# Optimization experiments

Measured on AMD Instinct MI355X. Metric: run time of the kernel, lower is better.

Reference implementation:

```python
import jax, jax.numpy as jnp
import numpy as np

SHRINKAGE = 0.1  # matches init_kwargs shrinkage_rate


def setup_inputs() -> dict:
    key = jax.random.key(0)
    k0, k1, k2, k3 = jax.random.split(key, 4)
    B, F, T, D, P = 8192, 256, 32, 6, 8
    N = 2 ** D - 1  # internal nodes per tree
    L = 2 ** D      # leaves per tree
    return {
        "x": jax.random.normal(k0, (B, F), dtype=jnp.float32),
        "W": jax.random.normal(k1, (T, N, F), dtype=jnp.float32) / np.float32(np.sqrt(F)),
        "b": jax.random.normal(k2, (T, N), dtype=jnp.float32) * 0.01,
        "phi": jax.random.normal(k3, (T, L, P), dtype=jnp.float32),
    }


def reference(x, W, b, phi):
    # x: [B,F]; W: [T,N,F]; b: [T,N]; phi: [T,L,P]
    T, N, F = W.shape
    L = N + 1
    D = int(round(np.log2(L)))
    # all node gating probabilities in one batched GEMM: p(right) per internal node
    s = jax.nn.sigmoid(jnp.einsum('bf,tnf->btn', x, W) + b)  # [B,T,N]
    # heap (level-order) node indexing: node at level d with prefix q has index 2^d-1+q;
    # leaf l's bit at level d is (l >> (D-1-d)) & 1 (1 -> right child -> prob s, 0 -> 1-s)
    leaves = np.arange(L)
    leaf_prob = jnp.ones(s.shape[:2] + (L,), dtype=s.dtype)  # [B,T,L]
    for d in range(D):  # static small loop over tree depth
        bits = jnp.asarray((leaves >> (D - 1 - d)) & 1, dtype=bool)
        idx = (2 ** d - 1) + (leaves >> (D - d))
        sd = s[:, :, idx]  # [B,T,L]
        leaf_prob = leaf_prob * jnp.where(bits, sd, 1.0 - sd)
    # per-tree prediction = sum_l path_prob_l * phi_l; GBM output = shrinkage * sum_t
    tree_pred = jnp.einsum('btl,tlp->btp', leaf_prob, phi)  # [B,T,P]
    return SHRINKAGE * tree_pred.sum(axis=1)  # [B,P]
```

## Files before the change

kernel.cpp:

```cpp
#include <hip/hip_runtime.h>

#define B_TOT   8192
#define F_DIM   256
#define T_TREES 32
#define N_NODES 63
#define P_DIM   8
#define BM      128
#define SHRINK  0.1f

typedef __bf16 bf16_t;
typedef bf16_t bf16x8 __attribute__((ext_vector_type(8)));
typedef float  f32x4  __attribute__((ext_vector_type(4)));
typedef unsigned short ushort8_t __attribute__((ext_vector_type(8)));
typedef unsigned short ushort4_t __attribute__((ext_vector_type(4)));

__device__ __forceinline__ unsigned short f2bf(float f) {
    unsigned int u = __float_as_uint(f);
    u += 0x7fffu + ((u >> 16) & 1u);
    return (unsigned short)(u >> 16);
}
__device__ __forceinline__ unsigned int pk2bf(float a, float b) {
    unsigned int ua = __float_as_uint(a); ua += 0x7fffu + ((ua >> 16) & 1u);
    unsigned int ub = __float_as_uint(b); ub += 0x7fffu + ((ub >> 16) & 1u);
    return (ua >> 16) | (ub & 0xffff0000u);
}
__device__ __forceinline__ void gl_lds16(const void* g, void* l) {
    __builtin_amdgcn_global_load_lds(
        (const __attribute__((address_space(1))) unsigned int*)g,
        (__attribute__((address_space(3))) unsigned int*)l, 16, 0, 0);
}

__global__ __launch_bounds__(256) void cvt_all(
    const float* __restrict__ x, const float* __restrict__ W,
    const float* __restrict__ phi,
    unsigned short* __restrict__ xb, unsigned short* __restrict__ Wb,
    unsigned short* __restrict__ phiB, float* __restrict__ out)
{
    const int bx  = blockIdx.x;
    const int tid = threadIdx.x;
    if (bx < 2048) {
        const int i = bx * 256 + tid;
        const float4 v = *(const float4*)&x[(size_t)i * 4];
        ushort4_t h;
        h.x = f2bf(v.x); h.y = f2bf(v.y); h.z = f2bf(v.z); h.w = f2bf(v.w);
        *(ushort4_t*)&xb[(size_t)i * 4] = h;
    } else if (bx < 2560) {
        const int i = (bx - 2048) * 256 + tid;
        const int tree = i >> 12;
        const int rem  = i & 4095;
        const int row  = rem >> 6;
        const int c4   = rem & 63;
        float4 v = make_float4(0.f, 0.f, 0.f, 0.f);
        if (row < N_NODES)
            v = *(const float4*)&W[((size_t)(tree * N_NODES + row)) * F_DIM + c4 * 4];
        ushort4_t h;
        h.x = f2bf(v.x); h.y = f2bf(v.y); h.z = f2bf(v.z); h.w = f2bf(v.w);
        *(ushort4_t*)&Wb[(size_t)i * 4] = h;
    } else if (bx < 2576) {
        const int i = (bx - 2560) * 256 + tid;
        const int tree = i >> 7;
        const int rem  = i & 127;
        const int k2   = rem >> 6;
        const int lane = rem & 63;
        const int lm   = lane & 15;
        const int quad = lane >> 4;
        ushort8_t h;
#pragma unroll
        for (int j = 0; j < 8; ++j) {
            float v = 0.f;
            if (lm < 8) v = phi[(size_t)tree * 512 + (k2 * 32 + quad * 8 + j) * 8 + lm];
            h[j] = f2bf(v);
        }
        *(ushort8_t*)&phiB[(size_t)i * 8] = h;
    } else {
        const int i = (bx - 2576) * 256 + tid;
        *(float4*)&out[(size_t)i * 4] = make_float4(0.f, 0.f, 0.f, 0.f);
    }
}

__global__ __launch_bounds__(256, 4) void softgbm_main(
    const unsigned short* __restrict__ xb, const unsigned short* __restrict__ Wb,
    const unsigned short* __restrict__ phiB, const float* __restrict__ bias,
    float* __restrict__ out)
{
    __shared__ union Smem {
        struct { unsigned short A[BM * 64]; unsigned short B[BM * 64]; } g;
        unsigned short ss[2 * BM * 64];
    } sm;
    __shared__ float bs2[2][64];

    const int tid  = threadIdx.x;
    const int tp   = blockIdx.x;
    const int b0   = blockIdx.y * BM;
    const int wave = tid >> 6;
    const int lane = tid & 63;
    const int quad = lane >> 4;
    const int lm   = lane & 15;
    const int wr   = wave >> 1;
    const int wc   = wave & 1;

    if (tid < 128) {
        const int p = tid >> 6, node = tid & 63;
        bs2[p][node] = (node < N_NODES) ? bias[(tp * 2 + p) * N_NODES + node] : 0.f;
    }

    f32x4 acc[4][4];
#pragma unroll
    for (int m = 0; m < 4; ++m)
#pragma unroll
        for (int n = 0; n < 4; ++n)
            acc[m][n] = f32x4{0.f, 0.f, 0.f, 0.f};

    for (int ko = 0; ko < F_DIM; ko += 64) {
        __syncthreads();
#pragma unroll
        for (int i = 0; i < 4; ++i) {
            const int r = wave * 32 + i * 8 + (lane >> 3);
            const int c = (lane & 7) ^ (r & 7);
            gl_lds16(&xb[(size_t)(b0 + r) * F_DIM + ko + c * 8],
                     &sm.g.A[(wave * 32 + i * 8) * 64]);
        }
#pragma unroll
        for (int i = 0; i < 4; ++i) {
            const int r = wave * 32 + i * 8 + (lane >> 3);
            const int c = (lane & 7) ^ (r & 7);
            gl_lds16(&Wb[(size_t)(tp * 128 + r) * F_DIM + ko + c * 8],
                     &sm.g.B[(wave * 32 + i * 8) * 64]);
        }
        __syncthreads();

#pragma unroll
        for (int ks = 0; ks < 2; ++ks) {
            bf16x8 af[4], bfr[4];
#pragma unroll
            for (int m = 0; m < 4; ++m) {
                const int r  = wr * 64 + m * 16 + lm;
                const int cp = (ks * 4 + quad) ^ (r & 7);
                af[m] = __builtin_bit_cast(bf16x8, *(ushort8_t*)&sm.g.A[r * 64 + cp * 8]);
            }
#pragma unroll
            for (int n = 0; n < 4; ++n) {
                const int r  = wc * 64 + n * 16 + lm;
                const int cp = (ks * 4 + quad) ^ (r & 7);
                bfr[n] = __builtin_bit_cast(bf16x8, *(ushort8_t*)&sm.g.B[r * 64 + cp * 8]);
            }
#pragma unroll
            for (int m = 0; m < 4; ++m)
#pragma unroll
                for (int n = 0; n < 4; ++n)
                    acc[m][n] = __builtin_amdgcn_mfma_f32_16x16x32_bf16(af[m], bfr[n], acc[m][n], 0, 0, 0);
        }
    }
    __syncthreads();

    bf16x8 pb[2][2];
#pragma unroll
    for (int p = 0; p < 2; ++p)
#pragma unroll
        for (int k2 = 0; k2 < 2; ++k2)
            pb[p][k2] = __builtin_bit_cast(bf16x8,
                *(const ushort8_t*)&phiB[(size_t)(((tp * 2 + p) * 2 + k2) * 64 + lane) * 8]);

    int slot[4];
#pragma unroll
    for (int n = 0; n < 4; ++n) {
        const int node = n * 16 + lm;
        const int np1  = node + 1;
        const int d    = 31 - __builtin_clz(np1);
        if (d == 0) slot[n] = 0;
        else {
            const int half = 1 << (d - 1);
            const int u    = np1 - (1 << d);
            const int hh   = (u >= half) ? 1 : 0;
            const int pos  = half + (u & (half - 1));
            slot[n] = hh * 32 + pos;
        }
    }

#pragma unroll
    for (int m = 0; m < 4; ++m)
#pragma unroll
        for (int n = 0; n < 4; ++n) {
            const int node = n * 16 + lm;
            const float bb = bs2[wc][node];
#pragma unroll
            for (int reg = 0; reg < 4; ++reg) {
                const int rr = wr * 64 + m * 16 + quad * 4 + reg;
                const float z = acc[m][n][reg] + bb;
                const unsigned short sv = f2bf(__frcp_rn(1.0f + __expf(-z)));
                if (node < N_NODES) {
                    unsigned short* base = &sm.ss[(wc * BM + rr) * 64];
                    base[slot[n]] = sv;
                    if (node == 0) base[32] = sv;
                }
            }
        }
    __syncthreads();

    const int row = tid >> 1;
    const int h   = tid & 1;
    const int rs  = row & 7;

    f32x4 accp[2] = { f32x4{0.f,0.f,0.f,0.f}, f32x4{0.f,0.f,0.f,0.f} };

    for (int p = 0; p < 2; ++p) {
        unsigned short* ssp = &sm.ss[p * (BM * 64)];
        unsigned int w[16];
        {
            const unsigned short* sp = &ssp[row * 64 + h * 32];
            *(uint4*)&w[0]  = *(const uint4*)&sp[0];
            *(uint4*)&w[4]  = *(const uint4*)&sp[8];
            *(uint4*)&w[8]  = *(const uint4*)&sp[16];
            *(uint4*)&w[12] = *(const uint4*)&sp[24];
        }
#define VAL(j) ((j) & 1 ? __uint_as_float(w[(j) >> 1] & 0xffff0000u) \
                        : __uint_as_float(w[(j) >> 1] << 16))
        const float s0 = VAL(0);
        const float q1 = h ? s0 : (1.0f - s0);
        float q2[2], q3[4], q4[8], q5[16];
        {
            const float tv = VAL(1);
            q2[1] = q1 * tv; q2[0] = q1 - q2[1];
        }
#pragma unroll
        for (int v = 0; v < 2; ++v) {
            const float tv = VAL(2 + v);
            q3[2 * v + 1] = q2[v] * tv; q3[2 * v] = q2[v] - q3[2 * v + 1];
        }
#pragma unroll
        for (int v = 0; v < 4; ++v) {
            const float tv = VAL(4 + v);
            q4[2 * v + 1] = q3[v] * tv; q4[2 * v] = q3[v] - q4[2 * v + 1];
        }
#pragma unroll
        for (int v = 0; v < 8; ++v) {
            const float tv = VAL(8 + v);
            q5[2 * v + 1] = q4[v] * tv; q5[2 * v] = q4[v] - q5[2 * v + 1];
        }
#pragma unroll
        for (int i = 0; i < 4; ++i) {
            float q6[8];
#pragma unroll
            for (int v = 0; v < 4; ++v) {
                const float tv = VAL(16 + i * 4 + v);
                q6[2 * v + 1] = q5[i * 4 + v] * tv;
                q6[2 * v]     = q5[i * 4 + v] - q6[2 * v + 1];
            }
            uint4 wv;
            wv.x = pk2bf(q6[0], q6[1]);
            wv.y = pk2bf(q6[2], q6[3]);
            wv.z = pk2bf(q6[4], q6[5]);
            wv.w = pk2bf(q6[6], q6[7]);
            *(uint4*)&ssp[row * 64 + ((h * 4 + i) ^ rs) * 8] = wv;
        }
#undef VAL

#pragma unroll
        for (int mg = 0; mg < 2; ++mg)
#pragma unroll
            for (int k2 = 0; k2 < 2; ++k2) {
                const int r2 = wave * 32 + mg * 16 + lm;
                const int cp = (k2 * 4 + quad) ^ (r2 & 7);
                const bf16x8 afr = __builtin_bit_cast(bf16x8,
                    *(ushort8_t*)&ssp[r2 * 64 + cp * 8]);
                accp[mg] = __builtin_amdgcn_mfma_f32_16x16x32_bf16(afr, pb[p][k2], accp[mg], 0, 0, 0);
            }
    }

    if (lm < P_DIM) {
#pragma unroll
        for (int mg = 0; mg < 2; ++mg)
#pragma unroll
            for (int reg = 0; reg < 4; ++reg) {
                const int r2 = wave * 32 + mg * 16 + quad * 4 + reg;
                atomicAdd(&out[(size_t)(b0 + r2) * P_DIM + lm], SHRINK * accp[mg][reg]);
            }
    }
}

extern "C" void kernel_launch(void* const* d_in, const int* in_sizes, int n_in,
                              void* d_out, int out_size, void* d_ws, size_t ws_size,
                              hipStream_t stream) {
    const float* x    = (const float*)d_in[0];
    const float* W    = (const float*)d_in[1];
    const float* bias = (const float*)d_in[2];
    const float* phi  = (const float*)d_in[3];
    float* out = (float*)d_out;

    unsigned short* xb   = (unsigned short*)d_ws;
    unsigned short* Wb   = xb + (size_t)B_TOT * F_DIM;
    unsigned short* phiB = Wb + (size_t)T_TREES * 64 * F_DIM;

    cvt_all<<<dim3(2640), dim3(256), 0, stream>>>(x, W, phi, xb, Wb, phiB, out);

    dim3 grid(T_TREES / 2, B_TOT / BM);
    softgbm_main<<<grid, dim3(256), 0, stream>>>(xb, Wb, phiB, bias, out);
}
```

Measured before the change: 86.65 us.

## Split leaf-probability stage per wave by tree and row half, hoist phi loads

Each wave now builds leaf probabilities for its own tree (wc) and its own 64-row half (wr). Each thread expands the full 64-leaf tree for one row, replacing the old two-threads-per-row split and the slot remapping. Sigmoids are stored in plain heap order with an XOR swizzle, and the phi B-fragment load is moved ahead of the main GEMM so it overlaps. In exchange, each thread uses more registers, and the output atomics double because the two trees are no longer summed inside the block.

```diff
diff --git a/kernel.cpp b/kernel.cpp
--- a/kernel.cpp
+++ b/kernel.cpp
@@ -104,6 +104,12 @@
         bs2[p][node] = (node < N_NODES) ? bias[(tp * 2 + p) * N_NODES + node] : 0.f;
     }
 
+    bf16x8 pb[2];
+#pragma unroll
+    for (int k2 = 0; k2 < 2; ++k2)
+        pb[k2] = __builtin_bit_cast(bf16x8,
+            *(const ushort8_t*)&phiB[(size_t)(((tp * 2 + wc) * 2 + k2) * 64 + lane) * 8]);
+
     f32x4 acc[4][4];
 #pragma unroll
     for (int m = 0; m < 4; ++m)
@@ -153,30 +159,6 @@
     }
     __syncthreads();
 
-    bf16x8 pb[2][2];
-#pragma unroll
-    for (int p = 0; p < 2; ++p)
-#pragma unroll
-        for (int k2 = 0; k2 < 2; ++k2)
-            pb[p][k2] = __builtin_bit_cast(bf16x8,
-                *(const ushort8_t*)&phiB[(size_t)(((tp * 2 + p) * 2 + k2) * 64 + lane) * 8]);
-
-    int slot[4];
-#pragma unroll
-    for (int n = 0; n < 4; ++n) {
-        const int node = n * 16 + lm;
-        const int np1  = node + 1;
-        const int d    = 31 - __builtin_clz(np1);
-        if (d == 0) slot[n] = 0;
-        else {
-            const int half = 1 << (d - 1);
-            const int u    = np1 - (1 << d);
-            const int hh   = (u >= half) ? 1 : 0;
-            const int pos  = half + (u & (half - 1));
-            slot[n] = hh * 32 + pos;
-        }
-    }
-
 #pragma unroll
     for (int m = 0; m < 4; ++m)
 #pragma unroll
@@ -188,91 +170,86 @@
                 const int rr = wr * 64 + m * 16 + quad * 4 + reg;
                 const float z = acc[m][n][reg] + bb;
                 const unsigned short sv = f2bf(__frcp_rn(1.0f + __expf(-z)));
-                if (node < N_NODES) {
-                    unsigned short* base = &sm.ss[(wc * BM + rr) * 64];
-                    base[slot[n]] = sv;
-                    if (node == 0) base[32] = sv;
-                }
+                if (node < N_NODES)
+                    sm.ss[(wc * BM + rr) * 64 + ((node >> 3) ^ (rr & 7)) * 8 + (node & 7)] = sv;
             }
         }
     __syncthreads();
 
-    const int row = tid >> 1;
-    const int h   = tid & 1;
+    const int row = wr * 64 + lane;
     const int rs  = row & 7;
-
-    f32x4 accp[2] = { f32x4{0.f,0.f,0.f,0.f}, f32x4{0.f,0.f,0.f,0.f} };
-
-    for (int p = 0; p < 2; ++p) {
-        unsigned short* ssp = &sm.ss[p * (BM * 64)];
-        unsigned int w[16];
-        {
-            const unsigned short* sp = &ssp[row * 64 + h * 32];
-            *(uint4*)&w[0]  = *(const uint4*)&sp[0];
-            *(uint4*)&w[4]  = *(const uint4*)&sp[8];
-            *(uint4*)&w[8]  = *(const uint4*)&sp[16];
-            *(uint4*)&w[12] = *(const uint4*)&sp[24];
-        }
+    unsigned short* srow = &sm.ss[(wc * BM + row) * 64];
+
+    unsigned int w[32];
+#pragma unroll
+    for (int c = 0; c < 8; ++c)
+        *(uint4*)&w[c * 4] = *(const uint4*)&srow[(c ^ rs) * 8];
+
 #define VAL(j) ((j) & 1 ? __uint_as_float(w[(j) >> 1] & 0xffff0000u) \
                         : __uint_as_float(w[(j) >> 1] << 16))
+    float q1[2], q2[4], q3[8], q4[16], q5[32];
+    {
         const float s0 = VAL(0);
-        const float q1 = h ? s0 : (1.0f - s0);
-        float q2[2], q3[4], q4[8], q5[16];
-        {
-            const float tv = VAL(1);
-            q2[1] = q1 * tv; q2[0] = q1 - q2[1];
-        }
-#pragma unroll
-        for (int v = 0; v < 2; ++v) {
-            const float tv = VAL(2 + v);
-            q3[2 * v + 1] = q2[v] * tv; q3[2 * v] = q2[v] - q3[2 * v + 1];
-        }
+        q1[1] = s0; q1[0] = 1.0f - s0;
+    }
+#pragma unroll
+    for (int v = 0; v < 2; ++v) {
+        const float tv = VAL(1 + v);
+        q2[2 * v + 1] = q1[v] * tv; q2[2 * v] = q1[v] - q2[2 * v + 1];
+    }
+#pragma unroll
+    for (int v = 0; v < 4; ++v) {
+        const float tv = VAL(3 + v);
+        q3[2 * v + 1] = q2[v] * tv; q3[2 * v] = q2[v] - q3[2 * v + 1];
+    }
+#pragma unroll
+    for (int v = 0; v < 8; ++v) {
+        const float tv = VAL(7 + v);
+        q4[2 * v + 1] = q3[v] * tv; q4[2 * v] = q3[v] - q4[2 * v + 1];
+    }
+#pragma unroll
+    for (int v = 0; v < 16; ++v) {
+        const float tv = VAL(15 + v);
+        q5[2 * v + 1] = q4[v] * tv; q5[2 * v] = q4[v] - q5[2 * v + 1];
+    }
+#pragma unroll
+    for (int i = 0; i < 8; ++i) {
+        float q6[8];
 #pragma unroll
         for (int v = 0; v < 4; ++v) {
-            const float tv = VAL(4 + v);
-            q4[2 * v + 1] = q3[v] * tv; q4[2 * v] = q3[v] - q4[2 * v + 1];
-        }
-#pragma unroll
-        for (int v = 0; v < 8; ++v) {
-            const float tv = VAL(8 + v);
-            q5[2 * v + 1] = q4[v] * tv; q5[2 * v] = q4[v] - q5[2 * v + 1];
-        }
-#pragma unroll
-        for (int i = 0; i < 4; ++i) {
-            float q6[8];
-#pragma unroll
-            for (int v = 0; v < 4; ++v) {
-                const float tv = VAL(16 + i * 4 + v);
-                q6[2 * v + 1] = q5[i * 4 + v] * tv;
-                q6[2 * v]     = q5[i * 4 + v] - q6[2 * v + 1];
-            }
-            uint4 wv;
-            wv.x = pk2bf(q6[0], q6[1]);
-            wv.y = pk2bf(q6[2], q6[3]);
-            wv.z = pk2bf(q6[4], q6[5]);
-            wv.w = pk2bf(q6[6], q6[7]);
-            *(uint4*)&ssp[row * 64 + ((h * 4 + i) ^ rs) * 8] = wv;
-        }
+            const float tv = VAL(31 + i * 4 + v);
+            q6[2 * v + 1] = q5[i * 4 + v] * tv;
+            q6[2 * v]     = q5[i * 4 + v] - q6[2 * v + 1];
+        }
+        uint4 wv;
+        wv.x = pk2bf(q6[0], q6[1]);
+        wv.y = pk2bf(q6[2], q6[3]);
+        wv.z = pk2bf(q6[4], q6[5]);
+        wv.w = pk2bf(q6[6], q6[7]);
+        *(uint4*)&srow[(i ^ rs) * 8] = wv;
+    }
 #undef VAL
 
-#pragma unroll
-        for (int mg = 0; mg < 2; ++mg)
-#pragma unroll
-            for (int k2 = 0; k2 < 2; ++k2) {
-                const int r2 = wave * 32 + mg * 16 + lm;
-                const int cp = (k2 * 4 + quad) ^ (r2 & 7);
-                const bf16x8 afr = __builtin_bit_cast(bf16x8,
-                    *(ushort8_t*)&ssp[r2 * 64 + cp * 8]);
-                accp[mg] = __builtin_amdgcn_mfma_f32_16x16x32_bf16(afr, pb[p][k2], accp[mg], 0, 0, 0);
-            }
-    }
+    f32x4 accp[4];
+#pragma unroll
+    for (int mg = 0; mg < 4; ++mg) accp[mg] = f32x4{0.f, 0.f, 0.f, 0.f};
+#pragma unroll
+    for (int mg = 0; mg < 4; ++mg)
+#pragma unroll
+        for (int k2 = 0; k2 < 2; ++k2) {
+            const int r2 = wr * 64 + mg * 16 + lm;
+            const int cp = (k2 * 4 + quad) ^ (r2 & 7);
+            const bf16x8 afr = __builtin_bit_cast(bf16x8,
+                *(ushort8_t*)&sm.ss[(wc * BM + r2) * 64 + cp * 8]);
+            accp[mg] = __builtin_amdgcn_mfma_f32_16x16x32_bf16(afr, pb[k2], accp[mg], 0, 0, 0);
+        }
 
     if (lm < P_DIM) {
 #pragma unroll
-        for (int mg = 0; mg < 2; ++mg)
+        for (int mg = 0; mg < 4; ++mg)
 #pragma unroll
             for (int reg = 0; reg < 4; ++reg) {
-                const int r2 = wave * 32 + mg * 16 + quad * 4 + reg;
+                const int r2 = wr * 64 + mg * 16 + quad * 4 + reg;
                 atomicAdd(&out[(size_t)(b0 + r2) * P_DIM + lm], SHRINK * accp[mg][reg]);
             }
     }
```

After: 91.56 us. 1.06x slower.
